# Kernel optimization log

Hardware: AMD Instinct MI355X
Metric: run time of the kernel (lower is better)

The kernel has to match this reference:

```python
import jax, jax.numpy as jnp
import numpy as np

EMBED_DIM = 768
NUM_HEADS = 8
HEAD_DIM = EMBED_DIM // NUM_HEADS  # 96
SCALE = HEAD_DIM ** -0.5


def setup_inputs() -> dict:
    key = jax.random.key(0)
    k1, k2, k3 = jax.random.split(key, 3)
    x = jax.random.normal(k1, (2, 4096, EMBED_DIM), dtype=jnp.float32)
    # nn.Linear weights stored [out, in]; init scaled like kaiming-uniform-ish
    w_qkv = jax.random.normal(k2, (3 * EMBED_DIM, EMBED_DIM), dtype=jnp.float32) * (EMBED_DIM ** -0.5)
    w_proj = jax.random.normal(k3, (EMBED_DIM, EMBED_DIM), dtype=jnp.float32) * (EMBED_DIM ** -0.5)
    return {"x": x, "w_qkv": w_qkv, "w_proj": w_proj}


def reference(x, w_qkv, w_proj):
    B, N, C = x.shape
    H, D = NUM_HEADS, C // NUM_HEADS
    qkv = jnp.einsum('bnc,oc->bno', x, w_qkv)          # [B,N,3C]
    qkv = qkv.reshape(B, N, 3, H, D).transpose(2, 0, 3, 1, 4)  # [3,B,H,N,D]
    q, k, v = qkv[0], qkv[1], qkv[2]
    attn = jnp.einsum('bhnd,bhmd->bhnm', q, k) * SCALE  # [B,H,N,N]
    attn = jax.nn.softmax(attn, axis=-1)
    out = jnp.einsum('bhnm,bhmd->bhnd', attn, v)        # [B,H,N,D]
    out = out.transpose(0, 2, 1, 3).reshape(B, N, C)
    out = jnp.einsum('bnc,oc->bno', out, w_proj)        # proj (no bias)
    return out  # dropout p=0.0 -> identity
```

## Files before the change

kernel.cpp:

```cpp
#include <hip/hip_runtime.h>

typedef __bf16 bf16;
typedef __attribute__((ext_vector_type(8))) __bf16 bf16x8;
typedef __attribute__((ext_vector_type(2))) __bf16 bf16x2;
typedef __attribute__((ext_vector_type(4))) float f32x4;
typedef __attribute__((ext_vector_type(16))) float f32x16;
typedef __attribute__((ext_vector_type(8))) unsigned short ushort8;
typedef __attribute__((ext_vector_type(4))) unsigned short ushort4v;

__device__ __forceinline__ unsigned short f2bf(float f) {
    union { float f; unsigned int u; } v; v.f = f;
    unsigned int u = v.u;
    return (unsigned short)((u + 0x7fffu + ((u >> 16) & 1u)) >> 16);
}

#if __has_builtin(__builtin_amdgcn_cvt_pk_bf16_f32)
__device__ __forceinline__ unsigned int pk2bf(float a, float b) {
    union { bf16x2 v; unsigned int u; } c;
    c.v = __builtin_amdgcn_cvt_pk_bf16_f32(a, b);
    return c.u;
}
#else
__device__ __forceinline__ unsigned int pk2bf(float a, float b) {
    return (unsigned int)f2bf(a) | ((unsigned int)f2bf(b) << 16);
}
#endif

__device__ __forceinline__ f32x4 mfma16(bf16x8 a, bf16x8 b, f32x4 c) {
    return __builtin_amdgcn_mfma_f32_16x16x32_bf16(a, b, c, 0, 0, 0);
}
__device__ __forceinline__ f32x16 mfma32(bf16x8 a, bf16x8 b, f32x16 c) {
    return __builtin_amdgcn_mfma_f32_32x32x16_bf16(a, b, c, 0, 0, 0);
}

#if __has_builtin(__builtin_amdgcn_global_load_lds)
__device__ __forceinline__ void gload16(const unsigned short* g, unsigned short* l) {
    typedef const unsigned int __attribute__((address_space(1)))* gp_t;
    typedef unsigned int __attribute__((address_space(3)))* lp_t;
    __builtin_amdgcn_global_load_lds((gp_t)(const void*)g, (lp_t)(void*)l, 16, 0, 0);
}
#define GLL_LANE 1
#else
#define GLL_LANE 0
#endif

__global__ void cvt3_f32_bf16(const float* __restrict__ x, const float* __restrict__ wq,
                              const float* __restrict__ wp,
                              unsigned short* __restrict__ xb, unsigned short* __restrict__ wqb,
                              unsigned short* __restrict__ wpb) {
    int i = blockIdx.x * 256 + threadIdx.x;
    const float* in; unsigned short* out; int base;
    if (i < 1572864)      { in = x;  out = xb;  base = i; }
    else if (i < 2015232) { in = wq; out = wqb; base = i - 1572864; }
    else if (i < 2162688) { in = wp; out = wpb; base = i - 2015232; }
    else return;
    float4 f = reinterpret_cast<const float4*>(in)[base];
    union { ushort4v v; unsigned int u[2]; } o;
    o.u[0] = pk2bf(f.x, f.y);
    o.u[1] = pk2bf(f.z, f.w);
    reinterpret_cast<ushort4v*>(out)[base] = o.v;
}

__device__ __forceinline__ int kperm(int k5) {
    return (k5 & 3) | (((k5 >> 3) & 1) << 2) | (((k5 >> 4) & 1) << 3) | (((k5 >> 2) & 1) << 4);
}
__device__ __forceinline__ int kperm_inv(int p5) {
    return (p5 & 3) | (((p5 >> 4) & 1) << 2) | (((p5 >> 2) & 1) << 3) | (((p5 >> 3) & 1) << 4);
}

__global__ __launch_bounds__(256) void qkv_gemm(const unsigned short* __restrict__ A,
                                                const unsigned short* __restrict__ W,
                                                unsigned short* __restrict__ Qf,
                                                unsigned short* __restrict__ Kf,
                                                unsigned short* __restrict__ Vf) {
    __shared__ __align__(16) char smem[34816];
    unsigned short* As = (unsigned short*)smem;
    unsigned short* Bs = (unsigned short*)(smem + 8192);
    unsigned short* T  = (unsigned short*)smem;
    const int t = threadIdx.x;
    const int w = t >> 6, l = t & 63;
    const int wm = (w >> 1) * 64, wn = (w & 1) * 64;
    const int lr = l & 15, lq = l >> 4;
    const int m0 = blockIdx.y * 128, n0 = blockIdx.x * 128;
    f32x4 acc[4][4] = {};
    for (int k0 = 0; k0 < 768; k0 += 32) {
        __syncthreads();
#pragma unroll
        for (int i = 0; i < 2; ++i) {
            int v = t + i * 256;
            int r = v >> 2, c8 = (v & 3) * 8;
#if GLL_LANE
            gload16(&A[(m0 + r) * 768 + k0 + c8], &As[(w * 64 + i * 256) * 8]);
            gload16(&W[(n0 + r) * 768 + k0 + c8], &Bs[(w * 64 + i * 256) * 8]);
#else
            *reinterpret_cast<ushort8*>(&As[r * 32 + c8]) =
                *reinterpret_cast<const ushort8*>(&A[(m0 + r) * 768 + k0 + c8]);
            *reinterpret_cast<ushort8*>(&Bs[r * 32 + c8]) =
                *reinterpret_cast<const ushort8*>(&W[(n0 + r) * 768 + k0 + c8]);
#endif
        }
        __syncthreads();
        bf16x8 af[4], bfr[4];
#pragma unroll
        for (int mt = 0; mt < 4; ++mt)
            af[mt] = *reinterpret_cast<const bf16x8*>(&As[(wm + mt * 16 + lr) * 32 + lq * 8]);
#pragma unroll
        for (int nt = 0; nt < 4; ++nt)
            bfr[nt] = *reinterpret_cast<const bf16x8*>(&Bs[(wn + nt * 16 + lr) * 32 + lq * 8]);
#pragma unroll
        for (int mt = 0; mt < 4; ++mt)
#pragma unroll
            for (int nt = 0; nt < 4; ++nt)
                acc[mt][nt] = mfma16(af[mt], bfr[nt], acc[mt][nt]);
    }
    const int tsel = n0 / 768;
    __syncthreads();
    if (tsel < 2) {
#pragma unroll
        for (int nt = 0; nt < 4; ++nt)
#pragma unroll
            for (int mt = 0; mt < 4; ++mt)
#pragma unroll
                for (int r = 0; r < 4; ++r) {
                    int row = wm + mt * 16 + lq * 4 + r;
                    int col = wn + nt * 16 + lr;
                    float val = acc[mt][nt][r];
                    if (tsel == 0) val *= 0.14724444f;
                    T[row * 136 + col] = f2bf(val);
                }
    } else {
#pragma unroll
        for (int nt = 0; nt < 4; ++nt)
#pragma unroll
            for (int mt = 0; mt < 4; ++mt)
#pragma unroll
                for (int r = 0; r < 4; ++r) {
                    int row = wm + mt * 16 + lq * 4 + r;
                    int col = wn + nt * 16 + lr;
                    T[col * 136 + row] = f2bf(acc[mt][nt][r]);
                }
    }
    __syncthreads();
    if (tsel < 2) {
#pragma unroll
        for (int i = 0; i < 8; ++i) {
            int idx = t + i * 256;
            int pos31 = idx & 31;
            int rest = idx >> 5;
            int c8 = rest & 15, qg = rest >> 4;
            int l31 = (tsel == 1) ? kperm_inv(pos31) : pos31;
            int gncol = n0 + c8 * 8;
            int rem = gncol - tsel * 768;
            int head = rem / 96, d = rem - head * 96;
            int kq = d >> 4, h2 = (d >> 3) & 1;
            int gm = m0 + qg * 32 + l31;
            int b = gm >> 12, nn = gm & 4095;
            int bh = b * 8 + head;
            long chunk = (long)(bh * 128 + (nn >> 5)) * 6 + kq;
            ushort8 v8 = *reinterpret_cast<const ushort8*>(&T[(qg * 32 + l31) * 136 + c8 * 8]);
            unsigned short* dst = (tsel == 0) ? Qf : Kf;
            *reinterpret_cast<ushort8*>(&dst[(chunk << 9) + ((h2 * 32 + pos31) << 3)]) = v8;
        }
    } else {
#pragma unroll
        for (int i = 0; i < 8; ++i) {
            int idx = t + i * 256;
            int dl = idx & 31;
            int rr = idx >> 5;
            int r8 = rr & 15, cmb = rr >> 4;
            int col = cmb * 32 + dl;
            int gncol = n0 + col;
            int rem = gncol - 1536;
            int head = rem / 96, d = rem - head * 96;
            int dn = d >> 5;
            int keybase = m0 + r8 * 8;
            int b = keybase >> 12, nn = keybase & 4095;
            int kg = nn >> 5, f = (nn >> 4) & 1, hv = (nn >> 3) & 1;
            int bh = b * 8 + head;
            long chunk = (long)(bh * 128 + kg) * 6 + dn * 2 + f;
            ushort8 v8 = *reinterpret_cast<const ushort8*>(&T[col * 136 + r8 * 8]);
            *reinterpret_cast<ushort8*>(&Vf[(chunk << 9) + ((hv * 32 + dl) << 3)]) = v8;
        }
    }
}

__global__ __launch_bounds__(256, 2) void attn_kernel(const unsigned short* __restrict__ Qf,
                                                      const unsigned short* __restrict__ Kf,
                                                      const unsigned short* __restrict__ Vf,
                                                      unsigned short* __restrict__ Og) {
    __shared__ __align__(16) float red[4608];
    const int t = threadIdx.x;
    const int w = t >> 6, l = t & 63;
    const int wr = w >> 1, wk = w & 1;
    const int l31 = l & 31, h = l >> 5;
    const int b0 = blockIdx.x;
    const int kk = b0 >> 3;
    const int bh = (b0 & 7) * 2 + (kk >> 5);
    const int q0 = (kk & 31) * 128;
    const int voff = l << 3;

    bf16x8 aq[2][6];
#pragma unroll
    for (int qn = 0; qn < 2; ++qn) {
        long qb = ((long)((bh * 128 + (q0 >> 5) + wr * 2 + qn) * 6)) << 9;
#pragma unroll
        for (int kq = 0; kq < 6; ++kq)
            aq[qn][kq] = *reinterpret_cast<const bf16x8*>(&Qf[qb + (kq << 9) + voff]);
    }

    bf16x8 ones8;
#pragma unroll
    for (int i = 0; i < 8; ++i) ones8[i] = (__bf16)1.0f;

    f32x16 acc[2][3] = {};
    f32x16 acc_l[2] = {};

    for (int it = 0; it < 64; ++it) {
        const int kt = wk * 64 + it;
        const long kbase = ((long)((bh * 128 + kt) * 6)) << 9;
        f32x16 s[2] = {};
#pragma unroll
        for (int kq = 0; kq < 6; ++kq) {
            bf16x8 bk = *reinterpret_cast<const bf16x8*>(&Kf[kbase + (kq << 9) + voff]);
            s[0] = mfma32(bk, aq[0][kq], s[0]);
            s[1] = mfma32(bk, aq[1][kq], s[1]);
        }
        union PF { unsigned int u[4]; bf16x8 v8; } p[2][2];
#pragma unroll
        for (int qn = 0; qn < 2; ++qn) {
            float e[16];
#pragma unroll
            for (int r = 0; r < 16; ++r) e[r] = __builtin_amdgcn_exp2f(s[qn][r]);
#pragma unroll
            for (int f = 0; f < 2; ++f) {
                p[qn][f].u[0] = pk2bf(e[4 * f + 0], e[4 * f + 1]);
                p[qn][f].u[1] = pk2bf(e[4 * f + 2], e[4 * f + 3]);
                p[qn][f].u[2] = pk2bf(e[8 + 4 * f + 0], e[8 + 4 * f + 1]);
                p[qn][f].u[3] = pk2bf(e[8 + 4 * f + 2], e[8 + 4 * f + 3]);
            }
        }
#pragma unroll
        for (int dn = 0; dn < 3; ++dn) {
#pragma unroll
            for (int f = 0; f < 2; ++f) {
                bf16x8 vb = *reinterpret_cast<const bf16x8*>(
                    &Vf[kbase + ((dn * 2 + f) << 9) + voff]);
                acc[0][dn] = mfma32(p[0][f].v8, vb, acc[0][dn]);
                acc[1][dn] = mfma32(p[1][f].v8, vb, acc[1][dn]);
            }
        }
#pragma unroll
        for (int qn = 0; qn < 2; ++qn)
#pragma unroll
            for (int f = 0; f < 2; ++f)
                acc_l[qn] = mfma32(p[qn][f].v8, ones8, acc_l[qn]);
    }

    const int rbase = (wr * 64 + l) * 36;
#pragma unroll
    for (int ps = 0; ps < 3; ++ps) {
        __syncthreads();
        if (wk == 1) {
#pragma unroll
            for (int c = 0; c < 2; ++c) {
                int c2 = ps * 2 + c, qn = c2 / 3, dn = c2 % 3;
#pragma unroll
                for (int u = 0; u < 4; ++u) {
                    f32x4 tmp;
#pragma unroll
                    for (int j = 0; j < 4; ++j) tmp[j] = acc[qn][dn][u * 4 + j];
                    *reinterpret_cast<f32x4*>(&red[rbase + c * 16 + u * 4]) = tmp;
                }
            }
        }
        __syncthreads();
        if (wk == 0) {
#pragma unroll
            for (int c = 0; c < 2; ++c) {
                int c2 = ps * 2 + c, qn = c2 / 3, dn = c2 % 3;
#pragma unroll
                for (int u = 0; u < 4; ++u) {
                    f32x4 tmp = *reinterpret_cast<const f32x4*>(&red[rbase + c * 16 + u * 4]);
#pragma unroll
                    for (int j = 0; j < 4; ++j) acc[qn][dn][u * 4 + j] += tmp[j];
                }
            }
        }
    }
    __syncthreads();
    if (wk == 1) {
#pragma unroll
        for (int qn = 0; qn < 2; ++qn)
#pragma unroll
            for (int u = 0; u < 4; ++u) {
                f32x4 tmp;
#pragma unroll
                for (int j = 0; j < 4; ++j) tmp[j] = acc_l[qn][u * 4 + j];
                *reinterpret_cast<f32x4*>(&red[rbase + qn * 16 + u * 4]) = tmp;
            }
    }
    __syncthreads();
    if (wk == 0) {
#pragma unroll
        for (int qn = 0; qn < 2; ++qn)
#pragma unroll
            for (int u = 0; u < 4; ++u) {
                f32x4 tmp = *reinterpret_cast<const f32x4*>(&red[rbase + qn * 16 + u * 4]);
#pragma unroll
                for (int j = 0; j < 4; ++j) acc_l[qn][u * 4 + j] += tmp[j];
            }
        const int b = bh >> 3, head = bh & 7;
#pragma unroll
        for (int qn = 0; qn < 2; ++qn) {
#pragma unroll
            for (int reg = 0; reg < 16; ++reg) {
                int qloc = (reg & 3) + 8 * (reg >> 2) + 4 * h;
                int n = q0 + wr * 64 + qn * 32 + qloc;
                float inv = 1.f / acc_l[qn][reg];
                int rowoff = (b * 4096 + n) * 768 + head * 96;
#pragma unroll
                for (int dn = 0; dn < 3; ++dn)
                    Og[rowoff + dn * 32 + l31] = f2bf(acc[qn][dn][reg] * inv);
            }
        }
    }
}

__global__ __launch_bounds__(256) void proj_gemm(const unsigned short* __restrict__ A,
                                                 const unsigned short* __restrict__ W,
                                                 float* __restrict__ out) {
    __shared__ __align__(16) unsigned short As[128 * 32];
    __shared__ __align__(16) unsigned short Bs[128 * 32];
    const int t = threadIdx.x;
    const int w = t >> 6, l = t & 63;
    const int wm = (w >> 1) * 64, wn = (w & 1) * 64;
    const int lr = l & 15, lq = l >> 4;
    const int m0 = blockIdx.y * 128, n0 = blockIdx.x * 128;
    f32x4 acc[4][4] = {};
    for (int k0 = 0; k0 < 768; k0 += 32) {
        __syncthreads();
#pragma unroll
        for (int i = 0; i < 2; ++i) {
            int v = t + i * 256;
            int r = v >> 2, c8 = (v & 3) * 8;
#if GLL_LANE
            gload16(&A[(m0 + r) * 768 + k0 + c8], &As[(w * 64 + i * 256) * 8]);
            gload16(&W[(n0 + r) * 768 + k0 + c8], &Bs[(w * 64 + i * 256) * 8]);
#else
            *reinterpret_cast<ushort8*>(&As[r * 32 + c8]) =
                *reinterpret_cast<const ushort8*>(&A[(m0 + r) * 768 + k0 + c8]);
            *reinterpret_cast<ushort8*>(&Bs[r * 32 + c8]) =
                *reinterpret_cast<const ushort8*>(&W[(n0 + r) * 768 + k0 + c8]);
#endif
        }
        __syncthreads();
        bf16x8 af[4], bfr[4];
#pragma unroll
        for (int mt = 0; mt < 4; ++mt)
            af[mt] = *reinterpret_cast<const bf16x8*>(&As[(wm + mt * 16 + lr) * 32 + lq * 8]);
#pragma unroll
        for (int nt = 0; nt < 4; ++nt)
            bfr[nt] = *reinterpret_cast<const bf16x8*>(&Bs[(wn + nt * 16 + lr) * 32 + lq * 8]);
#pragma unroll
        for (int mt = 0; mt < 4; ++mt)
#pragma unroll
            for (int nt = 0; nt < 4; ++nt)
                acc[mt][nt] = mfma16(af[mt], bfr[nt], acc[mt][nt]);
    }
#pragma unroll
    for (int nt = 0; nt < 4; ++nt) {
        int gn = n0 + wn + nt * 16 + lr;
#pragma unroll
        for (int mt = 0; mt < 4; ++mt) {
#pragma unroll
            for (int r = 0; r < 4; ++r) {
                int gm = m0 + wm + mt * 16 + lq * 4 + r;
                out[gm * 768 + gn] = acc[mt][nt][r];
            }
        }
    }
}

extern "C" void kernel_launch(void* const* d_in, const int* in_sizes, int n_in,
                              void* d_out, int out_size, void* d_ws, size_t ws_size,
                              hipStream_t stream) {
    const float* x     = (const float*)d_in[0];
    const float* wqkv  = (const float*)d_in[1];
    const float* wproj = (const float*)d_in[2];
    float* out = (float*)d_out;
    char* ws = (char*)d_ws;
    unsigned short* xb     = (unsigned short*)(ws);
    unsigned short* wqkvb  = (unsigned short*)(ws + 12582912);
    unsigned short* wprojb = (unsigned short*)(ws + 16121856);
    unsigned short* Qf     = (unsigned short*)(ws + 17301504);
    unsigned short* Kf     = (unsigned short*)(ws + 29884416);
    unsigned short* Vf     = (unsigned short*)(ws + 42467328);
    unsigned short* attnb  = xb;

    cvt3_f32_bf16<<<8448, 256, 0, stream>>>(x, wqkv, wproj, xb, wqkvb, wprojb);
    qkv_gemm<<<dim3(18, 64), 256, 0, stream>>>(xb, wqkvb, Qf, Kf, Vf);
    attn_kernel<<<512, 256, 0, stream>>>(Qf, Kf, Vf, attnb);
    proj_gemm<<<dim3(6, 64), 256, 0, stream>>>(attnb, wprojb, out);
}
```

Baseline: 274.8 us.

## Software-pipeline QK^T with softmax/PV and compute row sums on VALU

Each iteration now computes the next key tile's QK^T scores while applying exp and the PV MFMAs to the current tile, using double-buffered score registers so matrix and vector work can overlap. The ones-vector MFMA used to accumulate softmax denominators is replaced by scalar fp32 sums of the exp values, combined across half-waves with a shuffle and across waves through shared memory. This removes four MFMAs per iteration but adds VALU adds and register pressure. The wrapped last prefetch computes one extra unused tile, and the sums now come from unrounded fp32 values rather than the bf16-rounded probabilities.

```diff
diff --git a/kernel.cpp b/kernel.cpp
--- a/kernel.cpp
+++ b/kernel.cpp
@@ -208,53 +208,72 @@
             aq[qn][kq] = *reinterpret_cast<const bf16x8*>(&Qf[qb + (kq << 9) + voff]);
     }
 
-    bf16x8 ones8;
-#pragma unroll
-    for (int i = 0; i < 8; ++i) ones8[i] = (__bf16)1.0f;
-
     f32x16 acc[2][3] = {};
-    f32x16 acc_l[2] = {};
-
-    for (int it = 0; it < 64; ++it) {
-        const int kt = wk * 64 + it;
-        const long kbase = ((long)((bh * 128 + kt) * 6)) << 9;
-        f32x16 s[2] = {};
+    float lsum0 = 0.f, lsum1 = 0.f;
+
+    f32x16 sA[2], sB[2];
+    long kb_cur = ((long)((bh * 128 + wk * 64) * 6)) << 9;
+    {
+#pragma unroll
+        for (int z = 0; z < 16; ++z) { sA[0][z] = 0.f; sA[1][z] = 0.f; }
 #pragma unroll
         for (int kq = 0; kq < 6; ++kq) {
-            bf16x8 bk = *reinterpret_cast<const bf16x8*>(&Kf[kbase + (kq << 9) + voff]);
-            s[0] = mfma32(bk, aq[0][kq], s[0]);
-            s[1] = mfma32(bk, aq[1][kq], s[1]);
-        }
-        union PF { unsigned int u[4]; bf16x8 v8; } p[2][2];
-#pragma unroll
-        for (int qn = 0; qn < 2; ++qn) {
-            float e[16];
-#pragma unroll
-            for (int r = 0; r < 16; ++r) e[r] = __builtin_amdgcn_exp2f(s[qn][r]);
-#pragma unroll
-            for (int f = 0; f < 2; ++f) {
-                p[qn][f].u[0] = pk2bf(e[4 * f + 0], e[4 * f + 1]);
-                p[qn][f].u[1] = pk2bf(e[4 * f + 2], e[4 * f + 3]);
-                p[qn][f].u[2] = pk2bf(e[8 + 4 * f + 0], e[8 + 4 * f + 1]);
-                p[qn][f].u[3] = pk2bf(e[8 + 4 * f + 2], e[8 + 4 * f + 3]);
-            }
-        }
-#pragma unroll
-        for (int dn = 0; dn < 3; ++dn) {
-#pragma unroll
-            for (int f = 0; f < 2; ++f) {
-                bf16x8 vb = *reinterpret_cast<const bf16x8*>(
-                    &Vf[kbase + ((dn * 2 + f) << 9) + voff]);
-                acc[0][dn] = mfma32(p[0][f].v8, vb, acc[0][dn]);
-                acc[1][dn] = mfma32(p[1][f].v8, vb, acc[1][dn]);
-            }
-        }
-#pragma unroll
-        for (int qn = 0; qn < 2; ++qn)
-#pragma unroll
-            for (int f = 0; f < 2; ++f)
-                acc_l[qn] = mfma32(p[qn][f].v8, ones8, acc_l[qn]);
-    }
+            bf16x8 bk = *reinterpret_cast<const bf16x8*>(&Kf[kb_cur + (kq << 9) + voff]);
+            sA[0] = mfma32(bk, aq[0][kq], sA[0]);
+            sA[1] = mfma32(bk, aq[1][kq], sA[1]);
+        }
+    }
+
+#define ATTN_STEP(SCUR, SNXT, IT)                                                          \
+    {                                                                                      \
+        const int kt_n = wk * 64 + (((IT) + 1) & 63);                                      \
+        const long kb_n = ((long)((bh * 128 + kt_n) * 6)) << 9;                            \
+        _Pragma("unroll")                                                                  \
+        for (int z = 0; z < 16; ++z) { SNXT[0][z] = 0.f; SNXT[1][z] = 0.f; }               \
+        _Pragma("unroll")                                                                  \
+        for (int kq = 0; kq < 6; ++kq) {                                                   \
+            bf16x8 bk = *reinterpret_cast<const bf16x8*>(&Kf[kb_n + (kq << 9) + voff]);    \
+            SNXT[0] = mfma32(bk, aq[0][kq], SNXT[0]);                                      \
+            SNXT[1] = mfma32(bk, aq[1][kq], SNXT[1]);                                      \
+        }                                                                                  \
+        union PF { unsigned int u[4]; bf16x8 v8; } p[2][2];                                \
+        _Pragma("unroll")                                                                  \
+        for (int qn = 0; qn < 2; ++qn) {                                                   \
+            float e[16];                                                                   \
+            _Pragma("unroll")                                                              \
+            for (int r = 0; r < 16; ++r) e[r] = __builtin_amdgcn_exp2f(SCUR[qn][r]);       \
+            float s0 = (e[0] + e[1]) + (e[2] + e[3]);                                      \
+            float s1 = (e[4] + e[5]) + (e[6] + e[7]);                                      \
+            float s2 = (e[8] + e[9]) + (e[10] + e[11]);                                    \
+            float s3 = (e[12] + e[13]) + (e[14] + e[15]);                                  \
+            if (qn == 0) lsum0 += (s0 + s1) + (s2 + s3);                                   \
+            else         lsum1 += (s0 + s1) + (s2 + s3);                                   \
+            _Pragma("unroll")                                                              \
+            for (int f = 0; f < 2; ++f) {                                                  \
+                p[qn][f].u[0] = pk2bf(e[4 * f + 0], e[4 * f + 1]);                         \
+                p[qn][f].u[1] = pk2bf(e[4 * f + 2], e[4 * f + 3]);                         \
+                p[qn][f].u[2] = pk2bf(e[8 + 4 * f + 0], e[8 + 4 * f + 1]);                 \
+                p[qn][f].u[3] = pk2bf(e[8 + 4 * f + 2], e[8 + 4 * f + 3]);                 \
+            }                                                                              \
+        }                                                                                  \
+        _Pragma("unroll")                                                                  \
+        for (int dn = 0; dn < 3; ++dn) {                                                   \
+            _Pragma("unroll")                                                              \
+            for (int f = 0; f < 2; ++f) {                                                  \
+                bf16x8 vb = *reinterpret_cast<const bf16x8*>(                              \
+                    &Vf[kb_cur + ((dn * 2 + f) << 9) + voff]);                             \
+                acc[0][dn] = mfma32(p[0][f].v8, vb, acc[0][dn]);                           \
+                acc[1][dn] = mfma32(p[1][f].v8, vb, acc[1][dn]);                           \
+            }                                                                              \
+        }                                                                                  \
+        kb_cur = kb_n;                                                                     \
+    }
+
+    for (int it2 = 0; it2 < 32; ++it2) {
+        ATTN_STEP(sA, sB, it2 * 2)
+        ATTN_STEP(sB, sA, it2 * 2 + 1)
+    }
+#undef ATTN_STEP
 
     const int rbase = (wr * 64 + l) * 36;
 #pragma unroll
@@ -287,28 +306,21 @@
             }
         }
     }
+
+    lsum0 += __shfl_xor(lsum0, 32);
+    lsum1 += __shfl_xor(lsum1, 32);
     __syncthreads();
-    if (wk == 1) {
-#pragma unroll
-        for (int qn = 0; qn < 2; ++qn)
-#pragma unroll
-            for (int u = 0; u < 4; ++u) {
-                f32x4 tmp;
-#pragma unroll
-                for (int j = 0; j < 4; ++j) tmp[j] = acc_l[qn][u * 4 + j];
-                *reinterpret_cast<f32x4*>(&red[rbase + qn * 16 + u * 4]) = tmp;
-            }
+    if (wk == 1 && h == 0) {
+        red[(wr * 2 + 0) * 32 + l31] = lsum0;
+        red[(wr * 2 + 1) * 32 + l31] = lsum1;
+    }
+    __syncthreads();
+    if (wk == 0 && h == 0) {
+        red[128 + (wr * 2 + 0) * 32 + l31] = 1.f / (lsum0 + red[(wr * 2 + 0) * 32 + l31]);
+        red[128 + (wr * 2 + 1) * 32 + l31] = 1.f / (lsum1 + red[(wr * 2 + 1) * 32 + l31]);
     }
     __syncthreads();
     if (wk == 0) {
-#pragma unroll
-        for (int qn = 0; qn < 2; ++qn)
-#pragma unroll
-            for (int u = 0; u < 4; ++u) {
-                f32x4 tmp = *reinterpret_cast<const f32x4*>(&red[rbase + qn * 16 + u * 4]);
-#pragma unroll
-                for (int j = 0; j < 4; ++j) acc_l[qn][u * 4 + j] += tmp[j];
-            }
         const int b = bh >> 3, head = bh & 7;
 #pragma unroll
         for (int qn = 0; qn < 2; ++qn) {
@@ -316,7 +328,7 @@
             for (int reg = 0; reg < 16; ++reg) {
                 int qloc = (reg & 3) + 8 * (reg >> 2) + 4 * h;
                 int n = q0 + wr * 64 + qn * 32 + qloc;
-                float inv = 1.f / acc_l[qn][reg];
+                float inv = red[128 + (wr * 2 + qn) * 32 + qloc];
                 int rowoff = (b * 4096 + n) * 768 + head * 96;
 #pragma unroll
                 for (int dn = 0; dn < 3; ++dn)
```

Result: slower. 358.4 us (+30.4%).
